# Kernel tuning notes

Hardware: AMD Instinct MI355X
Metric: run time of the kernel (lower is better)

Reference implementation:

```python
import jax, jax.numpy as jnp
import numpy as np

EPS = 1e-12  # matches torch F.normalize default eps


def setup_inputs() -> dict:
    key = jax.random.key(0)
    ks = jax.random.split(key, 8)
    B, N, D, H = 8, 2048, 128, 128
    s = 1.0 / np.sqrt(D)
    return {
        "x": jax.random.normal(ks[0], (B, N, D), dtype=jnp.float32),
        "edge_weight": jax.random.uniform(ks[1], (B, N, N), dtype=jnp.float32),
        "W0": jax.random.normal(ks[2], (D, H), dtype=jnp.float32) * s,
        "b0": jnp.zeros((H,), dtype=jnp.float32),
        "W1": jax.random.normal(ks[3], (H, H), dtype=jnp.float32) * s,
        "b1": jnp.zeros((H,), dtype=jnp.float32),
        "W2": jax.random.normal(ks[4], (H, H), dtype=jnp.float32) * s,
        "b2": jnp.zeros((H,), dtype=jnp.float32),
    }


def _adapt_conv(h, edge_weight, W, b, is_last):
    h = h @ W + b                                   # [B,N,H]
    norm = jnp.linalg.norm(h, axis=-1, keepdims=True)
    nh = h / jnp.maximum(norm, EPS)                 # L2 normalize (F.normalize)
    cos = jnp.einsum('bij,bkj->bik', nh, nh)        # [B,N,N] cosine similarity
    ew = edge_weight * cos                          # elementwise mask
    h = jnp.einsum('bpq,bqc->bpc', ew, h)           # weighted aggregation
    if not is_last:
        h = jax.nn.relu(h)                          # dropout p=0.0 -> identity
    return h


def reference(x, edge_weight, W0, b0, W1, b1, W2, b2):
    params = [(W0, b0), (W1, b1), (W2, b2)]
    h = x
    n_layers = len(params)
    for i, (W, b) in enumerate(params):
        h = _adapt_conv(h, edge_weight, W, b, is_last=(i == n_layers - 1))
    return h
```

## Files before the change

kernel.cpp:

```cpp
#include <hip/hip_runtime.h>
#include <hip/hip_bf16.h>
#include <math.h>


typedef __attribute__((ext_vector_type(8)))  short bf16x8;
typedef __attribute__((ext_vector_type(4)))  short bf16x4;
typedef __attribute__((ext_vector_type(4)))  float f32x4;
typedef __attribute__((ext_vector_type(16))) float f32x16;
typedef __attribute__((ext_vector_type(2)))  unsigned u32x2;

static constexpr int kB = 8, kN = 2048, kH = 128;

static __device__ __forceinline__ ushort bf16bits(float f) {
    __hip_bfloat16 hb = __float2bfloat16(f);
    return *reinterpret_cast<ushort*>(&hb);
}
static __device__ __forceinline__ unsigned pk2(float lo, float hi) {
    return (unsigned)bf16bits(lo) | ((unsigned)bf16bits(hi) << 16);
}
static __device__ __forceinline__ float bf2f_lo(unsigned u) {
    unsigned v = u << 16; float f; __builtin_memcpy(&f, &v, 4); return f;
}
static __device__ __forceinline__ float bf2f_hi(unsigned u) {
    unsigned v = u & 0xffff0000u; float f; __builtin_memcpy(&f, &v, 4); return f;
}

#define LDS_BARRIER()                                          \
    do {                                                       \
        asm volatile("s_waitcnt lgkmcnt(0)" ::: "memory");     \
        __builtin_amdgcn_s_barrier();                          \
        __builtin_amdgcn_sched_barrier(0);                     \
    } while (0)

__global__ __launch_bounds__(256) void cvt_bf16_kernel(
    const float* __restrict__ src, ushort* __restrict__ dst, int n4)
{
    int i = blockIdx.x * 256 + threadIdx.x;
    if (i >= n4) return;
    float4 v = ((const float4*)src)[i];
    bf16x4 o;
    o[0] = (short)bf16bits(v.x); o[1] = (short)bf16bits(v.y);
    o[2] = (short)bf16bits(v.z); o[3] = (short)bf16bits(v.w);
    ((bf16x4*)dst)[i] = o;
}

__global__ __launch_bounds__(256) void cvt_wT_kernel(
    const float* __restrict__ W0, const float* __restrict__ W1,
    const float* __restrict__ W2, ushort* __restrict__ WT)
{
    const float* W = blockIdx.y == 0 ? W0 : (blockIdx.y == 1 ? W1 : W2);
    int i = blockIdx.x * 256 + threadIdx.x;
    int d = i >> 7, c = i & 127;
    WT[(size_t)blockIdx.y * kH * kH + c * kH + d] = bf16bits(W[d * kH + c]);
}

__global__ __launch_bounds__(256) void linear_tr_kernel(
    const ushort* __restrict__ h16, const ushort* __restrict__ WT,
    const float* __restrict__ bias, ushort* __restrict__ tn16,
    ushort* __restrict__ tT16)
{
    __shared__ float ssb[64][2];
    __shared__ ushort tr[128 * 72];

    const int tid = threadIdx.x, lane = tid & 63, wid = tid >> 6;
    const int wr = wid >> 1, wc = wid & 1, quad = lane >> 4, l16 = lane & 15;
    const int rowbase = blockIdx.x * 64;
    const int b = rowbase / kN, q0 = rowbase % kN;

    f32x4 acc[2][4];
#pragma unroll
    for (int i = 0; i < 2; ++i)
#pragma unroll
        for (int ct = 0; ct < 4; ++ct) acc[i][ct] = (f32x4){0.f, 0.f, 0.f, 0.f};

#pragma unroll
    for (int k = 0; k < 4; ++k) {
        bf16x8 Af[2], Bf[4];
#pragma unroll
        for (int i = 0; i < 2; ++i)
            Af[i] = *(const bf16x8*)&h16[(size_t)(rowbase + wr * 32 + i * 16 + l16) * kH + k * 32 + quad * 8];
#pragma unroll
        for (int ct = 0; ct < 4; ++ct)
            Bf[ct] = *(const bf16x8*)&WT[(size_t)(wc * 64 + ct * 16 + l16) * kH + k * 32 + quad * 8];
#pragma unroll
        for (int i = 0; i < 2; ++i)
#pragma unroll
            for (int ct = 0; ct < 4; ++ct)
                acc[i][ct] = __builtin_amdgcn_mfma_f32_16x16x32_bf16(Af[i], Bf[ct], acc[i][ct], 0, 0, 0);
    }

    float bsr[4];
#pragma unroll
    for (int ct = 0; ct < 4; ++ct) bsr[ct] = bias[wc * 64 + ct * 16 + l16];

    f32x4 ss[2] = {(f32x4){0,0,0,0}, (f32x4){0,0,0,0}};
#pragma unroll
    for (int i = 0; i < 2; ++i)
#pragma unroll
        for (int ct = 0; ct < 4; ++ct)
#pragma unroll
            for (int r = 0; r < 4; ++r) {
                float v = acc[i][ct][r] + bsr[ct];
                acc[i][ct][r] = v;
                ss[i][r] += v * v;
            }
#pragma unroll
    for (int step = 1; step < 16; step <<= 1)
#pragma unroll
        for (int i = 0; i < 2; ++i)
#pragma unroll
            for (int r = 0; r < 4; ++r) ss[i][r] += __shfl_xor(ss[i][r], step);

    if (l16 == 0)
#pragma unroll
        for (int i = 0; i < 2; ++i)
#pragma unroll
            for (int r = 0; r < 4; ++r)
                ssb[wr * 32 + i * 16 + quad * 4 + r][wc] = ss[i][r];
    __syncthreads();

    float invr[2][4];
#pragma unroll
    for (int i = 0; i < 2; ++i)
#pragma unroll
        for (int r = 0; r < 4; ++r) {
            const int pl = wr * 32 + i * 16 + quad * 4 + r;
            float s2 = ssb[pl][0] + ssb[pl][1];
            invr[i][r] = 1.f / fmaxf(sqrtf(s2), 1e-12f);
        }

#pragma unroll
    for (int i = 0; i < 2; ++i)
#pragma unroll
        for (int ct = 0; ct < 4; ++ct)
#pragma unroll
            for (int r = 0; r < 4; ++r) {
                const int pl = wr * 32 + i * 16 + quad * 4 + r;
                const int c = wc * 64 + ct * 16 + l16;
                const float v = acc[i][ct][r];
                tn16[(size_t)(rowbase + pl) * kH + c] = bf16bits(v * invr[i][r]);
                tr[c * 72 + pl] = bf16bits(v);
            }
    __syncthreads();

    ushort* tTb = tT16 + (size_t)b * kH * kN;
#pragma unroll
    for (int it = 0; it < 4; ++it) {
        int idx = tid + 256 * it;
        int c = idx >> 3, ch = idx & 7;
        bf16x8 v = *(const bf16x8*)&tr[c * 72 + ch * 8];
        *(bf16x8*)&tTb[(size_t)c * kN + q0 + ch * 8] = v;
    }
}

__global__ __launch_bounds__(512, 2) void agg_kernel(
    const ushort* __restrict__ tn, const ushort* __restrict__ tT,
    const float* __restrict__ ew,
    ushort* __restrict__ hout, float* __restrict__ fout, int last)
{
    __shared__ char lds[147456];

    const int b = blockIdx.x, pbase = blockIdx.y * 64;
    const int tid = threadIdx.x, lane = tid & 63, wid = tid >> 6;
    const int wp = wid >> 2, wq = wid & 3;
    const int l31 = lane & 31, h = lane >> 5;

    const ushort* tb  = tn + (size_t)b * kN * kH;
    const ushort* tTb = tT + (size_t)b * kH * kN;
    const float*  ewb = ew + (size_t)b * kN * kN;

    char* TQ   = lds;
    char* TT   = lds + 65536;
    char* myEw = lds + 131072 + wid * 2048;

    const int pbg = pbase + wp * 32;

    bf16x8 tP[8];
#pragma unroll
    for (int m = 0; m < 8; ++m)
        tP[m] = *(const bf16x8*)&tb[(size_t)(pbg + l31) * kH + m * 16 + h * 8];

    f32x16 oacc[4];
#pragma unroll
    for (int ct = 0; ct < 4; ++ct)
#pragma unroll
        for (int r = 0; r < 16; ++r) oacc[ct][r] = 0.f;

    const int sgRow = tid >> 4, sgCh = tid & 15;
    const int ewR = lane >> 3, ewQ = lane & 7;

    bf16x8 rQ[4], rT[4];
    f32x4 eC[4];

    auto prefetch = [&](int qb) {
#pragma unroll
        for (int j = 0; j < 4; ++j) {
            rQ[j] = *(const bf16x8*)&tb[(size_t)(qb + sgRow + 32 * j) * kH + sgCh * 8];
            rT[j] = *(const bf16x8*)&tTb[(size_t)(sgRow + 32 * j) * kN + qb + sgCh * 8];
        }
#pragma unroll
        for (int j = 0; j < 4; ++j)
            eC[j] = *(const f32x4*)&ewb[(size_t)(pbg + 8 * j + ewR) * kN + qb + wq * 32 + ewQ * 4];
    };
    prefetch(0);

    auto buildFrags = [&](const f32x16& sa, const f32x16& sb, bf16x8* out2) {
        float sv[16];
#pragma unroll
        for (int g = 0; g < 4; ++g) {
            u32x2 ev = *(const u32x2*)&myEw[l31 * 64 + ((16 * g + 8 * h) ^ ((l31 & 7) << 3))];
            sv[4 * g + 0] = (sa[4 * g + 0] + sb[4 * g + 0]) * bf2f_lo(ev[0]);
            sv[4 * g + 1] = (sa[4 * g + 1] + sb[4 * g + 1]) * bf2f_hi(ev[0]);
            sv[4 * g + 2] = (sa[4 * g + 2] + sb[4 * g + 2]) * bf2f_lo(ev[1]);
            sv[4 * g + 3] = (sa[4 * g + 3] + sb[4 * g + 3]) * bf2f_hi(ev[1]);
        }
#pragma unroll
        for (int kk = 0; kk < 2; ++kk) {
            const int e0 = kk * 8;
            unsigned a0 = pk2(sv[e0 + 0], sv[e0 + 1]);
            unsigned a1 = pk2(sv[e0 + 2], sv[e0 + 3]);
            unsigned b0 = pk2(sv[e0 + 4], sv[e0 + 5]);
            unsigned b1 = pk2(sv[e0 + 6], sv[e0 + 7]);
            const unsigned ta0 = (unsigned)__shfl_xor((int)a0, 32);
            const unsigned ta1 = (unsigned)__shfl_xor((int)a1, 32);
            const unsigned tb0 = (unsigned)__shfl_xor((int)b0, 32);
            const unsigned tb1 = (unsigned)__shfl_xor((int)b1, 32);
            union { unsigned u[4]; bf16x8 v; } U;
            U.u[0] = h ? tb0 : a0;
            U.u[1] = h ? tb1 : a1;
            U.u[2] = h ? b0  : ta0;
            U.u[3] = h ? b1  : ta1;
            out2[kk] = U.v;
        }
    };

    for (int it = 0; it < 16; ++it) {
        const int sBase = (it & 1) * 32768;

#pragma unroll
        for (int j = 0; j < 4; ++j) {
            const int row = sgRow + 32 * j;
            const int swz = (row & 15) << 4;
            *(bf16x8*)&TQ[sBase + row * 256 + ((sgCh * 16) ^ swz)] = rQ[j];
            *(bf16x8*)&TT[sBase + row * 256 + ((sgCh * 16) ^ swz)] = rT[j];
        }
#pragma unroll
        for (int j = 0; j < 4; ++j) {
            const int row = 8 * j + ewR;
            u32x2 w;
            w[0] = pk2(eC[j][0], eC[j][1]);
            w[1] = pk2(eC[j][2], eC[j][3]);
            *(u32x2*)&myEw[row * 64 + ((ewQ * 8) ^ ((row & 7) << 3))] = w;
        }

        if (it < 15) prefetch((it + 1) * 128);

        LDS_BARRIER();

        f32x16 s0a, s0b;
#pragma unroll
        for (int r = 0; r < 16; ++r) { s0a[r] = 0.f; s0b[r] = 0.f; }
        const int qrow = wq * 32 + l31;
        const int qswz = (qrow & 15) << 4;
#pragma unroll
        for (int m = 0; m < 8; ++m) {
            bf16x8 a = *(const bf16x8*)&TQ[sBase + qrow * 256 + ((m * 32 + 16 * h) ^ qswz)];
            if (m & 1) s0b = __builtin_amdgcn_mfma_f32_32x32x16_bf16(a, tP[m], s0b, 0, 0, 0);
            else       s0a = __builtin_amdgcn_mfma_f32_32x32x16_bf16(a, tP[m], s0a, 0, 0, 0);
        }

        bf16x8 aw[2];
        buildFrags(s0a, s0b, aw);

#pragma unroll
        for (int kkt = 0; kkt < 2; ++kkt) {
#pragma unroll
            for (int ct = 0; ct < 4; ++ct) {
                const int crow = 32 * ct + l31;
                bf16x8 Bf = *(const bf16x8*)&TT[sBase + crow * 256 +
                              ((wq * 64 + kkt * 32 + 16 * h) ^ ((crow & 15) << 4))];
                oacc[ct] = __builtin_amdgcn_mfma_f32_32x32x16_bf16(aw[kkt], Bf, oacc[ct], 0, 0, 0);
            }
        }
    }

    __syncthreads();
    float* OL = (float*)lds;
#pragma unroll
    for (int w = 0; w < 4; ++w) {
        if (wq == w) {
#pragma unroll
            for (int ct = 0; ct < 4; ++ct)
#pragma unroll
                for (int r = 0; r < 16; ++r) {
                    const int pl = wp * 32 + (r & 3) + 8 * (r >> 2) + 4 * h;
                    const int idx = pl * 128 + 32 * ct + l31;
                    if (w == 0) OL[idx] = oacc[ct][r];
                    else        OL[idx] += oacc[ct][r];
                }
        }
        __syncthreads();
    }

    {
        const int p = tid >> 3, cb = (tid & 7) * 16;
        const size_t gbase = (size_t)b * kN * kH + (size_t)(pbase + p) * kH + cb;
        if (!last) {
#pragma unroll
            for (int u = 0; u < 2; ++u) {
                bf16x8 o;
#pragma unroll
                for (int k = 0; k < 8; ++k)
                    o[k] = (short)bf16bits(fmaxf(OL[p * 128 + cb + u * 8 + k], 0.f));
                *(bf16x8*)&hout[gbase + u * 8] = o;
            }
        } else {
#pragma unroll
            for (int u = 0; u < 4; ++u) {
                f32x4 o;
#pragma unroll
                for (int k = 0; k < 4; ++k)
                    o[k] = OL[p * 128 + cb + u * 4 + k];
                *(f32x4*)&fout[gbase + u * 4] = o;
            }
        }
    }
}

extern "C" void kernel_launch(void* const* d_in, const int* in_sizes, int n_in,
                              void* d_out, int out_size, void* d_ws, size_t ws_size,
                              hipStream_t stream) {
    const float* x  = (const float*)d_in[0];
    const float* ew = (const float*)d_in[1];
    const float* W0 = (const float*)d_in[2];
    const float* b0 = (const float*)d_in[3];
    const float* W1 = (const float*)d_in[4];
    const float* b1 = (const float*)d_in[5];
    const float* W2 = (const float*)d_in[6];
    const float* b2 = (const float*)d_in[7];
    const float* bias[3] = {b0, b1, b2};

    const size_t nBNH = (size_t)kB * kN * kH;
    ushort* h16  = (ushort*)d_ws;
    ushort* tn16 = h16 + nBNH;
    ushort* tT16 = tn16 + nBNH;
    ushort* WT   = tT16 + nBNH;
    float*  out  = (float*)d_out;

    cvt_bf16_kernel<<<(int)(nBNH / 4 + 255) / 256, 256, 0, stream>>>(x, h16, (int)(nBNH / 4));
    cvt_wT_kernel<<<dim3(64, 3), 256, 0, stream>>>(W0, W1, W2, WT);

    for (int layer = 0; layer < 3; ++layer) {
        linear_tr_kernel<<<kB * kN / 64, 256, 0, stream>>>(
            h16, WT + (size_t)layer * kH * kH, bias[layer], tn16, tT16);
        agg_kernel<<<dim3(kB, kN / 64), 512, 0, stream>>>(
            tn16, tT16, ew, h16, out, layer == 2 ? 1 : 0);
    }
}
```

Before: 314.7 us.

## Shrink aggregation blocks to 32 rows, single-buffer LDS, use permlane32 swap

The aggregation kernel now uses 256-thread blocks covering 32 output rows instead of 512 threads covering 64. It drops LDS double buffering, so each block needs about half the shared memory and can co-reside more, at the cost of a second barrier per iteration. Because each block holds half as many rows, every q-tile of tn/tT is reloaded by twice as many blocks. The half-wave exchange in fragment building becomes v_permlane32_swap instead of four shuffles plus selects. The linear kernel now stages the normalized output through LDS so tn16 is written with coalesced 16-byte stores.

```diff
diff --git a/kernel.cpp b/kernel.cpp
--- a/kernel.cpp
+++ b/kernel.cpp
@@ -61,6 +61,7 @@
 {
     __shared__ float ssb[64][2];
     __shared__ ushort tr[128 * 72];
+    __shared__ ushort trn[64 * 136];
 
     const int tid = threadIdx.x, lane = tid & 63, wid = tid >> 6;
     const int wr = wid >> 1, wc = wid & 1, quad = lane >> 4, l16 = lane & 15;
@@ -138,8 +139,8 @@
                 const int pl = wr * 32 + i * 16 + quad * 4 + r;
                 const int c = wc * 64 + ct * 16 + l16;
                 const float v = acc[i][ct][r];
-                tn16[(size_t)(rowbase + pl) * kH + c] = bf16bits(v * invr[i][r]);
                 tr[c * 72 + pl] = bf16bits(v);
+                trn[pl * 136 + c] = bf16bits(v * invr[i][r]);
             }
     __syncthreads();
 
@@ -151,18 +152,24 @@
         bf16x8 v = *(const bf16x8*)&tr[c * 72 + ch * 8];
         *(bf16x8*)&tTb[(size_t)c * kN + q0 + ch * 8] = v;
     }
-}
-
-__global__ __launch_bounds__(512, 2) void agg_kernel(
+#pragma unroll
+    for (int it = 0; it < 4; ++it) {
+        int idx = tid + 256 * it;
+        int p = idx >> 4, ch = idx & 15;
+        bf16x8 v = *(const bf16x8*)&trn[p * 136 + ch * 8];
+        *(bf16x8*)&tn16[(size_t)(rowbase + p) * kH + ch * 8] = v;
+    }
+}
+
+__global__ __launch_bounds__(256, 2) void agg_kernel(
     const ushort* __restrict__ tn, const ushort* __restrict__ tT,
     const float* __restrict__ ew,
     ushort* __restrict__ hout, float* __restrict__ fout, int last)
 {
-    __shared__ char lds[147456];
-
-    const int b = blockIdx.x, pbase = blockIdx.y * 64;
-    const int tid = threadIdx.x, lane = tid & 63, wid = tid >> 6;
-    const int wp = wid >> 2, wq = wid & 3;
+    __shared__ char lds[73728];
+
+    const int b = blockIdx.x, pbase = blockIdx.y * 32;
+    const int tid = threadIdx.x, lane = tid & 63, wq = tid >> 6;
     const int l31 = lane & 31, h = lane >> 5;
 
     const ushort* tb  = tn + (size_t)b * kN * kH;
@@ -170,15 +177,13 @@
     const float*  ewb = ew + (size_t)b * kN * kN;
 
     char* TQ   = lds;
-    char* TT   = lds + 65536;
-    char* myEw = lds + 131072 + wid * 2048;
-
-    const int pbg = pbase + wp * 32;
+    char* TT   = lds + 32768;
+    char* myEw = lds + 65536 + wq * 2048;
 
     bf16x8 tP[8];
 #pragma unroll
     for (int m = 0; m < 8; ++m)
-        tP[m] = *(const bf16x8*)&tb[(size_t)(pbg + l31) * kH + m * 16 + h * 8];
+        tP[m] = *(const bf16x8*)&tb[(size_t)(pbase + l31) * kH + m * 16 + h * 8];
 
     f32x16 oacc[4];
 #pragma unroll
@@ -189,18 +194,18 @@
     const int sgRow = tid >> 4, sgCh = tid & 15;
     const int ewR = lane >> 3, ewQ = lane & 7;
 
-    bf16x8 rQ[4], rT[4];
+    bf16x8 rQ[8], rT[8];
     f32x4 eC[4];
 
     auto prefetch = [&](int qb) {
 #pragma unroll
-        for (int j = 0; j < 4; ++j) {
-            rQ[j] = *(const bf16x8*)&tb[(size_t)(qb + sgRow + 32 * j) * kH + sgCh * 8];
-            rT[j] = *(const bf16x8*)&tTb[(size_t)(sgRow + 32 * j) * kN + qb + sgCh * 8];
+        for (int j = 0; j < 8; ++j) {
+            rQ[j] = *(const bf16x8*)&tb[(size_t)(qb + sgRow + 16 * j) * kH + sgCh * 8];
+            rT[j] = *(const bf16x8*)&tTb[(size_t)(sgRow + 16 * j) * kN + qb + sgCh * 8];
         }
 #pragma unroll
         for (int j = 0; j < 4; ++j)
-            eC[j] = *(const f32x4*)&ewb[(size_t)(pbg + 8 * j + ewR) * kN + qb + wq * 32 + ewQ * 4];
+            eC[j] = *(const f32x4*)&ewb[(size_t)(pbase + 8 * j + ewR) * kN + qb + wq * 32 + ewQ * 4];
     };
     prefetch(0);
 
@@ -221,28 +226,26 @@
             unsigned a1 = pk2(sv[e0 + 2], sv[e0 + 3]);
             unsigned b0 = pk2(sv[e0 + 4], sv[e0 + 5]);
             unsigned b1 = pk2(sv[e0 + 6], sv[e0 + 7]);
-            const unsigned ta0 = (unsigned)__shfl_xor((int)a0, 32);
-            const unsigned ta1 = (unsigned)__shfl_xor((int)a1, 32);
-            const unsigned tb0 = (unsigned)__shfl_xor((int)b0, 32);
-            const unsigned tb1 = (unsigned)__shfl_xor((int)b1, 32);
+            asm("v_permlane32_swap_b32 %0, %1" : "+v"(a0), "+v"(b0));
+            asm("v_permlane32_swap_b32 %0, %1" : "+v"(a1), "+v"(b1));
             union { unsigned u[4]; bf16x8 v; } U;
-            U.u[0] = h ? tb0 : a0;
-            U.u[1] = h ? tb1 : a1;
-            U.u[2] = h ? b0  : ta0;
-            U.u[3] = h ? b1  : ta1;
+            U.u[0] = a0;
+            U.u[1] = a1;
+            U.u[2] = b0;
+            U.u[3] = b1;
             out2[kk] = U.v;
         }
     };
 
     for (int it = 0; it < 16; ++it) {
-        const int sBase = (it & 1) * 32768;
-
-#pragma unroll
-        for (int j = 0; j < 4; ++j) {
-            const int row = sgRow + 32 * j;
+        const int qb = it * 128;
+
+#pragma unroll
+        for (int j = 0; j < 8; ++j) {
+            const int row = sgRow + 16 * j;
             const int swz = (row & 15) << 4;
-            *(bf16x8*)&TQ[sBase + row * 256 + ((sgCh * 16) ^ swz)] = rQ[j];
-            *(bf16x8*)&TT[sBase + row * 256 + ((sgCh * 16) ^ swz)] = rT[j];
+            *(bf16x8*)&TQ[row * 256 + ((sgCh * 16) ^ swz)] = rQ[j];
+            *(bf16x8*)&TT[row * 256 + ((sgCh * 16) ^ swz)] = rT[j];
         }
 #pragma unroll
         for (int j = 0; j < 4; ++j) {
@@ -253,7 +256,7 @@
             *(u32x2*)&myEw[row * 64 + ((ewQ * 8) ^ ((row & 7) << 3))] = w;
         }
 
-        if (it < 15) prefetch((it + 1) * 128);
+        if (it < 15) prefetch(qb + 128);
 
         LDS_BARRIER();
 
@@ -264,7 +267,7 @@
         const int qswz = (qrow & 15) << 4;
 #pragma unroll
         for (int m = 0; m < 8; ++m) {
-            bf16x8 a = *(const bf16x8*)&TQ[sBase + qrow * 256 + ((m * 32 + 16 * h) ^ qswz)];
+            bf16x8 a = *(const bf16x8*)&TQ[qrow * 256 + ((m * 32 + 16 * h) ^ qswz)];
             if (m & 1) s0b = __builtin_amdgcn_mfma_f32_32x32x16_bf16(a, tP[m], s0b, 0, 0, 0);
             else       s0a = __builtin_amdgcn_mfma_f32_32x32x16_bf16(a, tP[m], s0a, 0, 0, 0);
         }
@@ -277,14 +280,14 @@
 #pragma unroll
             for (int ct = 0; ct < 4; ++ct) {
                 const int crow = 32 * ct + l31;
-                bf16x8 Bf = *(const bf16x8*)&TT[sBase + crow * 256 +
+                bf16x8 Bf = *(const bf16x8*)&TT[crow * 256 +
                               ((wq * 64 + kkt * 32 + 16 * h) ^ ((crow & 15) << 4))];
                 oacc[ct] = __builtin_amdgcn_mfma_f32_32x32x16_bf16(aw[kkt], Bf, oacc[ct], 0, 0, 0);
             }
         }
-    }
-
-    __syncthreads();
+        LDS_BARRIER();
+    }
+
     float* OL = (float*)lds;
 #pragma unroll
     for (int w = 0; w < 4; ++w) {
@@ -293,7 +296,7 @@
             for (int ct = 0; ct < 4; ++ct)
 #pragma unroll
                 for (int r = 0; r < 16; ++r) {
-                    const int pl = wp * 32 + (r & 3) + 8 * (r >> 2) + 4 * h;
+                    const int pl = (r & 3) + 8 * (r >> 2) + 4 * h;
                     const int idx = pl * 128 + 32 * ct + l31;
                     if (w == 0) OL[idx] = oacc[ct][r];
                     else        OL[idx] += oacc[ct][r];
@@ -353,7 +356,7 @@
     for (int layer = 0; layer < 3; ++layer) {
         linear_tr_kernel<<<kB * kN / 64, 256, 0, stream>>>(
             h16, WT + (size_t)layer * kH * kH, bias[layer], tn16, tT16);
-        agg_kernel<<<dim3(kB, kN / 64), 512, 0, stream>>>(
+        agg_kernel<<<dim3(kB, kN / 32), 256, 0, stream>>>(
             tn16, tT16, ew, h16, out, layer == 2 ? 1 : 0);
     }
 }
```

Result: slower. 353.7 us (+12.4%).
